# Optimization experiments

Measured on AMD Instinct MI355X. Metric: run time of the kernel, lower is better.

Reference implementation:

```python
import jax, jax.numpy as jnp
import numpy as np

H = 27  # hidden_size == input_size == num_classes


def _lstm_layer(x, h0, c0, Wih, Whh, bih, bhh):
    """One LSTM layer, batch_first input x: [B, T, H_in] -> [B, T, H].
    PyTorch gate order: i, f, g, o."""
    # Precompute input contribution for all timesteps: [B, T, 4H]
    xg = jnp.einsum('bti,gi->btg', x, Wih) + bih + bhh
    xg = jnp.transpose(xg, (1, 0, 2))  # [T, B, 4H] for scan over time

    def step(carry, xg_t):
        h, c = carry
        g = xg_t + h @ Whh.T  # [B, 4H]
        i, f, gg, o = jnp.split(g, 4, axis=-1)
        i = jax.nn.sigmoid(i)
        f = jax.nn.sigmoid(f)
        gg = jnp.tanh(gg)
        o = jax.nn.sigmoid(o)
        c = f * c + i * gg
        h = o * jnp.tanh(c)
        return (h, c), h

    _, hs = jax.lax.scan(step, (h0, c0), xg)  # hs: [T, B, H]
    return jnp.transpose(hs, (1, 0, 2))  # [B, T, H]


def setup_inputs() -> dict:
    key = jax.random.key(0)
    ks = jax.random.split(key, 9)
    B, T = 32768, 78
    s = 1.0 / np.sqrt(H)  # match PyTorch uniform(-1/sqrt(H),1/sqrt(H)) scale roughly
    return {
        'x': jax.random.normal(ks[0], (B, T, H), jnp.float32),
        'h0': jax.random.normal(ks[1], (3, B, H), jnp.float32),
        'c0': jax.random.normal(ks[2], (3, B, H), jnp.float32),
        'Wih': jax.random.normal(ks[3], (3, 4 * H, H), jnp.float32) * s,
        'Whh': jax.random.normal(ks[4], (3, 4 * H, H), jnp.float32) * s,
        'bih': jax.random.normal(ks[5], (3, 4 * H), jnp.float32) * s,
        'bhh': jax.random.normal(ks[6], (3, 4 * H), jnp.float32) * s,
        'Wl': jax.random.normal(ks[7], (H, H), jnp.float32) * s,
        'bl': jax.random.normal(ks[8], (H,), jnp.float32) * s,
    }


def reference(x, h0, c0, Wih, Whh, bih, bhh, Wl, bl):
    out = x
    for l in range(3):  # fixed num_layers=3
        out = _lstm_layer(out, h0[l], c0[l], Wih[l], Whh[l], bih[l], bhh[l])
    out = out.reshape(-1, H)  # [B*T, 27]
    return out @ Wl.T + bl
```

## Files before the change

kernel.cpp:

```cpp
#include <hip/hip_runtime.h>

#define H   27
#define H4  108
#define TT  78
#define NB  32768
#define LAYERS 3

__device__ __forceinline__ float fast_rcp(float x) { return __builtin_amdgcn_rcpf(x); }
__device__ __forceinline__ float fast_exp2(float x) { return __builtin_amdgcn_exp2f(x); }

#define LOG2E 1.4426950408889634f

__launch_bounds__(256, 2)
__global__ void lstm3_fused(const float* __restrict__ x,
                            const float* __restrict__ h0,
                            const float* __restrict__ c0,
                            const float* __restrict__ Wih,
                            const float* __restrict__ Whh,
                            const float* __restrict__ bih,
                            const float* __restrict__ bhh,
                            const float* __restrict__ Wl,
                            const float* __restrict__ bl,
                            float* __restrict__ out)
{
    __shared__ float xbuf[H * 65];
    __shared__ float hbuf[LAYERS][H * 64];
    __shared__ float gbuf[H4 * 64];
    __shared__ float obuf[H * 65];

    const int tid   = threadIdx.x;
    const int w     = __builtin_amdgcn_readfirstlane(tid >> 6);
    const int lane  = tid & 63;
    const int bbase = blockIdx.x * 64;

    const float e1 = (w == 2) ? (-2.f * LOG2E) : (-LOG2E);
    const float s2 = (w == 2) ?  2.f : 1.f;
    const float s0 = (w == 2) ? -1.f : 0.f;

    const int jbeg = w * 7;
    const int jcnt = (w == 3) ? 6 : 7;

    for (int e = tid; e < LAYERS * 64 * H; e += 256) {
        int l  = e / (64 * H);
        int r  = e - l * (64 * H);
        int bi = r / H;
        int k  = r - bi * H;
        hbuf[l][k * 64 + bi] = h0[(size_t)l * NB * H + (size_t)(bbase + bi) * H + k];
    }
    float c[LAYERS][7];
    #pragma unroll
    for (int l = 0; l < LAYERS; ++l) {
        #pragma unroll
        for (int jj = 0; jj < 7; ++jj) {
            int j = jbeg + jj;
            c[l][jj] = (jj < jcnt)
                     ? c0[(size_t)l * NB * H + (size_t)(bbase + lane) * H + j] : 0.f;
        }
    }
    __syncthreads();

    for (int t = 0; t < TT; ++t) {
        for (int e = tid; e < 64 * H; e += 256) {
            int bi = e / H;
            int k  = e - bi * H;
            xbuf[k * 65 + bi] = x[((size_t)(bbase + bi) * TT + t) * H + k];
        }
        __syncthreads();

        #pragma unroll
        for (int l = 0; l < LAYERS; ++l) {
            float xr[H], hr[H];
            const float* xin = (l == 0) ? xbuf : &hbuf[l - 1][0];
            const int    xs  = (l == 0) ? 65 : 64;
            #pragma unroll
            for (int k = 0; k < H; ++k) {
                xr[k] = xin[k * xs + lane];
                hr[k] = hbuf[l][k * 64 + lane];
            }

            const float* wi = Wih + ((size_t)l * H4 + w * H) * H;
            const float* wh = Whh + ((size_t)l * H4 + w * H) * H;
            const float* b1 = bih + l * H4 + w * H;
            const float* b2 = bhh + l * H4 + w * H;

            #pragma unroll 2
            for (int jr = 0; jr < H; ++jr) {
                float a = b1[jr] + b2[jr];
                #pragma unroll
                for (int k = 0; k < H; ++k) a += wi[jr * H + k] * xr[k];
                #pragma unroll
                for (int k = 0; k < H; ++k) a += wh[jr * H + k] * hr[k];
                a = s0 + s2 * fast_rcp(1.f + fast_exp2(e1 * a));
                gbuf[(w * H + jr) * 64 + lane] = a;
            }
            __syncthreads();

            #pragma unroll
            for (int jj = 0; jj < 7; ++jj) {
                if (jj < jcnt) {
                    int j = jbeg + jj;
                    float ig = gbuf[(0 * H + j) * 64 + lane];
                    float fg = gbuf[(1 * H + j) * 64 + lane];
                    float gg = gbuf[(2 * H + j) * 64 + lane];
                    float og = gbuf[(3 * H + j) * 64 + lane];
                    float cn = fg * c[l][jj] + ig * gg;
                    c[l][jj] = cn;
                    float th = -1.f + 2.f * fast_rcp(1.f + fast_exp2(-2.f * LOG2E * cn));
                    hbuf[l][j * 64 + lane] = og * th;
                }
            }
            __syncthreads();
        }

        {
            float h2[H];
            #pragma unroll
            for (int k = 0; k < H; ++k) h2[k] = hbuf[2][k * 64 + lane];
            #pragma unroll
            for (int jj = 0; jj < 7; ++jj) {
                if (jj < jcnt) {
                    int j = jbeg + jj;
                    float a = bl[j];
                    #pragma unroll
                    for (int k = 0; k < H; ++k) a += Wl[j * H + k] * h2[k];
                    obuf[j * 65 + lane] = a;
                }
            }
        }
        __syncthreads();

        for (int e = tid; e < 64 * H; e += 256) {
            int bi = e / H;
            int k  = e - bi * H;
            out[((size_t)(bbase + bi) * TT + t) * H + k] = obuf[k * 65 + bi];
        }
        __syncthreads();
    }
}

extern "C" void kernel_launch(void* const* d_in, const int* in_sizes, int n_in,
                              void* d_out, int out_size, void* d_ws, size_t ws_size,
                              hipStream_t stream) {
    (void)in_sizes; (void)n_in; (void)ws_size; (void)d_ws; (void)out_size;
    const float* x   = (const float*)d_in[0];
    const float* h0  = (const float*)d_in[1];
    const float* c0  = (const float*)d_in[2];
    const float* Wih = (const float*)d_in[3];
    const float* Whh = (const float*)d_in[4];
    const float* bih = (const float*)d_in[5];
    const float* bhh = (const float*)d_in[6];
    const float* Wl  = (const float*)d_in[7];
    const float* bl  = (const float*)d_in[8];
    float* out = (float*)d_out;

    lstm3_fused<<<dim3(NB / 64), dim3(256), 0, stream>>>(
        x, h0, c0, Wih, Whh, bih, bhh, Wl, bl, out);
}
```

Measured before the change: 3.648 ms.

## Repartition LSTM work by hidden unit across nine waves with double-buffered state

Changes the work split from four waves (one per gate) to nine waves, each owning three hidden units and computing all four gates for them. The shared gate buffer and its barrier go away, and double-buffering the hidden state removes the trailing barrier at the end of each timestep. In exchange, each wave now computes every gate row for its units, and the block is larger with launch bounds asking for higher occupancy, which adds register pressure that could cause spills.

```diff
diff --git a/kernel.cpp b/kernel.cpp
--- a/kernel.cpp
+++ b/kernel.cpp
@@ -1,17 +1,22 @@
 #include <hip/hip_runtime.h>
 
-#define H   27
-#define H4  108
-#define TT  78
-#define NB  32768
+#define H      27
+#define H4     108
+#define TT     78
+#define NB     32768
 #define LAYERS 3
-
-__device__ __forceinline__ float fast_rcp(float x) { return __builtin_amdgcn_rcpf(x); }
-__device__ __forceinline__ float fast_exp2(float x) { return __builtin_amdgcn_exp2f(x); }
+#define WAVES  9
+#define BLOCK  (WAVES * 64)
+#define JPW    3
 
 #define LOG2E 1.4426950408889634f
 
-__launch_bounds__(256, 2)
+__device__ __forceinline__ float fast_rcp(float x)  { return __builtin_amdgcn_rcpf(x); }
+__device__ __forceinline__ float fast_exp2(float x) { return __builtin_amdgcn_exp2f(x); }
+__device__ __forceinline__ float sigm_f(float a) { return fast_rcp(1.f + fast_exp2(-LOG2E * a)); }
+__device__ __forceinline__ float tanh_f(float a) { return -1.f + 2.f * fast_rcp(1.f + fast_exp2(-2.f * LOG2E * a)); }
+
+__launch_bounds__(BLOCK, 4)
 __global__ void lstm3_fused(const float* __restrict__ x,
                             const float* __restrict__ h0,
                             const float* __restrict__ c0,
@@ -24,90 +29,79 @@
                             float* __restrict__ out)
 {
     __shared__ float xbuf[H * 65];
-    __shared__ float hbuf[LAYERS][H * 64];
-    __shared__ float gbuf[H4 * 64];
+    __shared__ float hbuf[2][LAYERS][H * 64];
     __shared__ float obuf[H * 65];
 
     const int tid   = threadIdx.x;
     const int w     = __builtin_amdgcn_readfirstlane(tid >> 6);
     const int lane  = tid & 63;
     const int bbase = blockIdx.x * 64;
+    const int jbeg  = w * JPW;
 
-    const float e1 = (w == 2) ? (-2.f * LOG2E) : (-LOG2E);
-    const float s2 = (w == 2) ?  2.f : 1.f;
-    const float s0 = (w == 2) ? -1.f : 0.f;
-
-    const int jbeg = w * 7;
-    const int jcnt = (w == 3) ? 6 : 7;
-
-    for (int e = tid; e < LAYERS * 64 * H; e += 256) {
+    for (int e = tid; e < LAYERS * 64 * H; e += BLOCK) {
         int l  = e / (64 * H);
         int r  = e - l * (64 * H);
         int bi = r / H;
         int k  = r - bi * H;
-        hbuf[l][k * 64 + bi] = h0[(size_t)l * NB * H + (size_t)(bbase + bi) * H + k];
+        hbuf[0][l][k * 64 + bi] = h0[(size_t)l * NB * H + (size_t)(bbase + bi) * H + k];
     }
-    float c[LAYERS][7];
+    float c[LAYERS][JPW];
     #pragma unroll
-    for (int l = 0; l < LAYERS; ++l) {
+    for (int l = 0; l < LAYERS; ++l)
         #pragma unroll
-        for (int jj = 0; jj < 7; ++jj) {
-            int j = jbeg + jj;
-            c[l][jj] = (jj < jcnt)
-                     ? c0[(size_t)l * NB * H + (size_t)(bbase + lane) * H + j] : 0.f;
-        }
-    }
+        for (int jj = 0; jj < JPW; ++jj)
+            c[l][jj] = c0[(size_t)l * NB * H + (size_t)(bbase + lane) * H + (jbeg + jj)];
     __syncthreads();
 
+    int cur = 0;
     for (int t = 0; t < TT; ++t) {
-        for (int e = tid; e < 64 * H; e += 256) {
+        for (int e = tid; e < 64 * H; e += BLOCK) {
             int bi = e / H;
             int k  = e - bi * H;
             xbuf[k * 65 + bi] = x[((size_t)(bbase + bi) * TT + t) * H + k];
         }
         __syncthreads();
+        const int nxt = cur ^ 1;
 
         #pragma unroll
         for (int l = 0; l < LAYERS; ++l) {
             float xr[H], hr[H];
-            const float* xin = (l == 0) ? xbuf : &hbuf[l - 1][0];
+            const float* xin = (l == 0) ? xbuf : &hbuf[nxt][l - 1][0];
             const int    xs  = (l == 0) ? 65 : 64;
             #pragma unroll
             for (int k = 0; k < H; ++k) {
                 xr[k] = xin[k * xs + lane];
-                hr[k] = hbuf[l][k * 64 + lane];
+                hr[k] = hbuf[cur][l][k * 64 + lane];
             }
 
-            const float* wi = Wih + ((size_t)l * H4 + w * H) * H;
-            const float* wh = Whh + ((size_t)l * H4 + w * H) * H;
-            const float* b1 = bih + l * H4 + w * H;
-            const float* b2 = bhh + l * H4 + w * H;
-
-            #pragma unroll 2
-            for (int jr = 0; jr < H; ++jr) {
-                float a = b1[jr] + b2[jr];
-                #pragma unroll
-                for (int k = 0; k < H; ++k) a += wi[jr * H + k] * xr[k];
-                #pragma unroll
-                for (int k = 0; k < H; ++k) a += wh[jr * H + k] * hr[k];
-                a = s0 + s2 * fast_rcp(1.f + fast_exp2(e1 * a));
-                gbuf[(w * H + jr) * 64 + lane] = a;
-            }
-            __syncthreads();
+            const float* wiL = Wih + (size_t)l * H4 * H;
+            const float* whL = Whh + (size_t)l * H4 * H;
+            const float* b1L = bih + l * H4;
+            const float* b2L = bhh + l * H4;
 
             #pragma unroll
-            for (int jj = 0; jj < 7; ++jj) {
-                if (jj < jcnt) {
-                    int j = jbeg + jj;
-                    float ig = gbuf[(0 * H + j) * 64 + lane];
-                    float fg = gbuf[(1 * H + j) * 64 + lane];
-                    float gg = gbuf[(2 * H + j) * 64 + lane];
-                    float og = gbuf[(3 * H + j) * 64 + lane];
-                    float cn = fg * c[l][jj] + ig * gg;
-                    c[l][jj] = cn;
-                    float th = -1.f + 2.f * fast_rcp(1.f + fast_exp2(-2.f * LOG2E * cn));
-                    hbuf[l][j * 64 + lane] = og * th;
+            for (int jj = 0; jj < JPW; ++jj) {
+                const int j = jbeg + jj;
+                float acc[4];
+                #pragma unroll
+                for (int g = 0; g < 4; ++g) {
+                    const int row = g * H + j;
+                    const float* wi = wiL + row * H;
+                    const float* wh = whL + row * H;
+                    float a = b1L[row] + b2L[row];
+                    #pragma unroll
+                    for (int k = 0; k < H; ++k) a += wi[k] * xr[k];
+                    #pragma unroll
+                    for (int k = 0; k < H; ++k) a += wh[k] * hr[k];
+                    acc[g] = a;
                 }
+                const float ig = sigm_f(acc[0]);
+                const float fg = sigm_f(acc[1]);
+                const float gg = tanh_f(acc[2]);
+                const float og = sigm_f(acc[3]);
+                const float cn = fg * c[l][jj] + ig * gg;
+                c[l][jj] = cn;
+                hbuf[nxt][l][j * 64 + lane] = og * tanh_f(cn);
             }
             __syncthreads();
         }
@@ -115,26 +109,24 @@
         {
             float h2[H];
             #pragma unroll
-            for (int k = 0; k < H; ++k) h2[k] = hbuf[2][k * 64 + lane];
+            for (int k = 0; k < H; ++k) h2[k] = hbuf[nxt][2][k * 64 + lane];
             #pragma unroll
-            for (int jj = 0; jj < 7; ++jj) {
-                if (jj < jcnt) {
-                    int j = jbeg + jj;
-                    float a = bl[j];
-                    #pragma unroll
-                    for (int k = 0; k < H; ++k) a += Wl[j * H + k] * h2[k];
-                    obuf[j * 65 + lane] = a;
-                }
+            for (int jj = 0; jj < JPW; ++jj) {
+                const int j = jbeg + jj;
+                float a = bl[j];
+                #pragma unroll
+                for (int k = 0; k < H; ++k) a += Wl[j * H + k] * h2[k];
+                obuf[j * 65 + lane] = a;
             }
         }
         __syncthreads();
 
-        for (int e = tid; e < 64 * H; e += 256) {
+        for (int e = tid; e < 64 * H; e += BLOCK) {
             int bi = e / H;
             int k  = e - bi * H;
             out[((size_t)(bbase + bi) * TT + t) * H + k] = obuf[k * 65 + bi];
         }
-        __syncthreads();
+        cur = nxt;
     }
 }
 
@@ -153,6 +145,6 @@
     const float* bl  = (const float*)d_in[8];
     float* out = (float*)d_out;
 
-    lstm3_fused<<<dim3(NB / 64), dim3(256), 0, stream>>>(
+    lstm3_fused<<<dim3(NB / 64), dim3(BLOCK), 0, stream>>>(
         x, h0, c0, Wih, Whh, bih, bhh, Wl, bl, out);
 }
```

Measured after the change: 5.057 ms. 38.6% more time.
